# Performance work log

Hardware: AMD Instinct MI355X
Metric: run time of the kernel (lower is better)

The kernel has to match this reference:

```python
import jax, jax.numpy as jnp
import numpy as np

B, L, F, P = 128, 256, 4, 4   # dialogs, dialog length, future/past links
IN, H, C = 1024, 256, 7
N = B * L


def _build_edges():
    # same structure as build_intra_graph: self-loop + F future + P past per node
    i = np.arange(L)
    ss, tt = [], []
    for d in range(-P, F + 1):
        j = i + d
        m = (j >= 0) & (j < L)
        ss.append(i[m]); tt.append(j[m])
    s = np.concatenate(ss); t = np.concatenate(tt)
    offs = (np.arange(B) * L)[:, None]
    S = (s[None, :] + offs).ravel()
    T = (t[None, :] + offs).ravel()
    return np.stack([S, T]).astype(np.int32)


def setup_inputs() -> dict:
    key = jax.random.key(0)
    ks = jax.random.split(key, 16)
    ei = _build_edges()
    speakers = np.asarray(jax.random.randint(ks[0], (N,), 0, 2), dtype=np.int32)
    rel = (speakers[ei[0]] * speakers[ei[1]]).astype(np.int32)
    sd_in = 1.0 / np.sqrt(IN)
    sd_h = 1.0 / np.sqrt(H)
    return {
        "input": jax.random.normal(ks[1], (N, IN), jnp.float32),
        "dialog_lengths": jnp.full((B,), L, jnp.int32),
        "speakers": jnp.asarray(speakers),
        "labels": jax.random.randint(ks[2], (N,), 0, C, jnp.int32),
        "edge_index": jnp.asarray(ei),
        "rel_type": jnp.asarray(rel),
        # RGCNConv(IN, H, num_relations=2): per-relation weight, root weight, bias
        "W_rgcn": jax.random.normal(ks[3], (2, IN, H), jnp.float32) * sd_in,
        "W_root": jax.random.normal(ks[4], (IN, H), jnp.float32) * sd_in,
        "b_rgcn": jax.random.normal(ks[5], (H,), jnp.float32) * 0.01,
        # GraphConv(H, H): lin_rel (on aggregated neighbors, with bias), lin_root (no bias)
        "W_rel": jax.random.normal(ks[6], (H, H), jnp.float32) * sd_h,
        "b_rel": jax.random.normal(ks[7], (H,), jnp.float32) * 0.01,
        "W_grt": jax.random.normal(ks[8], (H, H), jnp.float32) * sd_h,
        # skip_con: Linear(IN, H)
        "W_skip": jax.random.normal(ks[9], (IN, H), jnp.float32) * sd_in,
        "b_skip": jax.random.normal(ks[10], (H,), jnp.float32) * 0.01,
        # classify: Linear(H, C)
        "W_cls": jax.random.normal(ks[11], (H, C), jnp.float32) * sd_h,
        "b_cls": jax.random.normal(ks[12], (C,), jnp.float32) * 0.01,
    }


def reference(input, dialog_lengths, speakers, labels, edge_index, rel_type,
              W_rgcn, W_root, b_rgcn, W_rel, b_rel, W_grt,
              W_skip, b_skip, W_cls, b_cls):
    n = input.shape[0]
    src, dst = edge_index[0], edge_index[1]
    seg = jax.ops.segment_sum

    # --- RGCNConv: out_i = x_i @ W_root + b + sum_r mean_{j in N_r(i)} x_j @ W_r
    t = jnp.einsum('ni,rio->rno', input, W_rgcn)      # [2, N, H]
    msg = t[rel_type, src]                            # [E, H] relation-specific messages
    h = input @ W_root + b_rgcn
    for r in range(2):
        m = (rel_type == r).astype(input.dtype)       # [E]
        s = seg(msg * m[:, None], dst, num_segments=n)
        cnt = seg(m, dst, num_segments=n)
        h = h + s / jnp.maximum(cnt, 1.0)[:, None]    # mean aggregation per relation

    # --- GraphConv (aggr='add'): out_i = W_rel @ sum_j h_j + b_rel + W_grt @ h_i
    neigh = seg(h[src], dst, num_segments=n)          # [N, H]
    h2 = neigh @ W_rel + b_rel + h @ W_grt

    # --- skip connection + classifier
    out = (h2 + input @ W_skip + b_skip) @ W_cls + b_cls  # [N, C]

    # --- cross entropy (mean)
    logp = jax.nn.log_softmax(out, axis=-1)
    loss = -jnp.mean(jnp.take_along_axis(logp, labels[:, None].astype(jnp.int32), axis=1))
    return out, loss
```

## Files before the change

### kernel.cpp

```cpp
#include <hip/hip_runtime.h>

#define NN 32768
#define INF 1024
#define HF 256

typedef __bf16 bf16x8 __attribute__((ext_vector_type(8)));
typedef float f32x4 __attribute__((ext_vector_type(4)));
typedef unsigned short u16x8 __attribute__((ext_vector_type(8)));

__device__ __forceinline__ float bf2f(unsigned short u) {
  union { unsigned int i; float f; } v; v.i = ((unsigned int)u) << 16; return v.f;
}
__device__ __forceinline__ unsigned short f2bf(float f) {
  union { float f; unsigned int i; } v; v.f = f;
  unsigned int x = v.i;
  return (unsigned short)((x + 0x7fffu + ((x >> 16) & 1u)) >> 16);
}

__device__ __forceinline__ void ld_lds16(const unsigned short* g, unsigned short* l) {
  __builtin_amdgcn_global_load_lds(
      (__attribute__((address_space(1))) const unsigned int*)g,
      (__attribute__((address_space(3))) unsigned int*)l, 16, 0, 0);
}

__global__ __launch_bounds__(256)
void diagcn_prep(const float* __restrict__ x, const float* __restrict__ Wrgcn,
                 const float* __restrict__ Wroot, const float* __restrict__ Wskip,
                 const float* __restrict__ Wgrt, const float* __restrict__ Wrel,
                 unsigned short* __restrict__ Xbf, unsigned short* __restrict__ WbigT,
                 unsigned short* __restrict__ WsmT, float* __restrict__ loss) {
  int bid = blockIdx.x;
  if (bid < 32768) {
    if (bid == 0 && threadIdx.x == 0) loss[0] = 0.f;
    int idx = bid * 256 + threadIdx.x;
    float4 v = ((const float4*)x)[idx];
    ushort4 u; u.x = f2bf(v.x); u.y = f2bf(v.y); u.z = f2bf(v.z); u.w = f2bf(v.w);
    ((ushort4*)Xbf)[idx] = u;
    return;
  }
  __shared__ float tile[64 * 65];
  int tb = bid - 32768;
  const float* src;
  int k0, ncol0;
  unsigned short* dst;
  int ldd, nrow0;
  if (tb < 256) {
    int tn = tb >> 4, tk = tb & 15;
    int mat = tn >> 2;
    src = (mat == 0) ? Wrgcn : (mat == 1) ? (Wrgcn + 262144) : (mat == 2) ? Wroot : Wskip;
    k0 = tk * 64; ncol0 = (tn & 3) * 64;
    dst = WbigT; ldd = 1024; nrow0 = tn * 64;
  } else {
    int t2 = tb - 256;
    int tn = t2 >> 3, tk = t2 & 7;
    src = (tk < 4) ? Wgrt : Wrel;
    k0 = (tk & 3) * 64; ncol0 = tn * 64;
    dst = WsmT; ldd = 512; nrow0 = tn * 64;
  }
  int kdst0 = (tb < 256) ? k0 : (((tb - 256) & 7) * 64);
  int c = threadIdx.x & 63, rb = threadIdx.x >> 6;
#pragma unroll
  for (int it = 0; it < 16; ++it) {
    int r = rb + it * 4;
    tile[r * 65 + c] = src[(size_t)(k0 + r) * 256 + ncol0 + c];
  }
  __syncthreads();
  int kk = threadIdx.x & 63;
#pragma unroll
  for (int it = 0; it < 16; ++it) {
    int nn = rb + it * 4;
    dst[(size_t)(nrow0 + nn) * ldd + kdst0 + kk] = f2bf(tile[kk * 65 + nn]);
  }
}

__global__ __launch_bounds__(256)
void diagcn_gemm1(const unsigned short* __restrict__ A, const unsigned short* __restrict__ BT,
                  unsigned short* __restrict__ Y) {
  const int K = 1024;
  __shared__ unsigned short As[128 * 64];
  __shared__ unsigned short Bs[128 * 64];
  const int tid = threadIdx.x;
  const int w = tid >> 6, lane = tid & 63;
  const int wm = w >> 1, wn = w & 1;
  const int quad = lane >> 4, l15 = lane & 15;
  const int b = blockIdx.x;
  const int m0 = (((b & 7) << 5) + (b >> 6)) << 7;
  const int n0 = ((b >> 3) & 7) << 7;
  const int rowg = lane >> 3;
  const int kbsw = (lane & 7) ^ rowg;

  f32x4 acc[4][4] = {};
  const unsigned short* Abase = A + (size_t)m0 * K + kbsw * 8;
  const unsigned short* Bbase = BT + (size_t)n0 * K + kbsw * 8;

  for (int k0 = 0; k0 < K; k0 += 64) {
#pragma unroll
    for (int t = 0; t < 4; ++t) {
      int grp = w * 4 + t;
      int rl = grp * 8 + rowg;
      ld_lds16(Abase + (size_t)rl * K + k0, &As[grp * 512]);
      ld_lds16(Bbase + (size_t)rl * K + k0, &Bs[grp * 512]);
    }
    __syncthreads();
#pragma unroll
    for (int ks = 0; ks < 2; ++ks) {
      bf16x8 av[4], bv[4];
      int kb = ks * 4 + quad;
#pragma unroll
      for (int i = 0; i < 4; ++i) {
        int ra = wm * 64 + i * 16 + l15;
        int rb2 = wn * 64 + i * 16 + l15;
        av[i] = *(const bf16x8*)&As[ra * 64 + ((kb ^ (ra & 7)) << 3)];
        bv[i] = *(const bf16x8*)&Bs[rb2 * 64 + ((kb ^ (rb2 & 7)) << 3)];
      }
#pragma unroll
      for (int i = 0; i < 4; ++i)
#pragma unroll
        for (int j = 0; j < 4; ++j)
          acc[i][j] = __builtin_amdgcn_mfma_f32_16x16x32_bf16(av[i], bv[j], acc[i][j], 0, 0, 0);
    }
    __syncthreads();
  }
#pragma unroll
  for (int i = 0; i < 4; ++i)
#pragma unroll
    for (int j = 0; j < 4; ++j) {
      int row = m0 + wm * 64 + i * 16 + quad * 4;
      int col = n0 + wn * 64 + j * 16 + l15;
#pragma unroll
      for (int r = 0; r < 4; ++r)
        Y[(size_t)(row + r) * 1024 + col] = f2bf(acc[i][j][r]);
    }
}

__global__ __launch_bounds__(256)
void diagcn_h(const unsigned short* __restrict__ Y, const int* __restrict__ spk,
              const float* __restrict__ brgcn, unsigned short* __restrict__ A2) {
  int b = blockIdx.x;
  int wv = threadIdx.x >> 6, lane = threadIdx.x & 63;
  int half = lane >> 5, li = lane & 31, c0 = li << 3;
  int node = ((b & 7) << 12) + ((b >> 3) << 3) + wv * 2 + half;
  int p = node & 255, dbase = node - p;
  int si = spk[node];
  float a0[8] = {}, a1[8] = {};
  float n0 = 0.f, n1 = 0.f;
#pragma unroll
  for (int d = -4; d <= 4; ++d) {
    int pj = p + d;
    float w = (pj >= 0 && pj < 256) ? 1.f : 0.f;
    int jc = pj < 0 ? 0 : (pj > 255 ? 255 : pj);
    int nj = dbase + jc;
    int rel = si & spk[nj];
    u16x8 v = *(const u16x8*)&Y[(size_t)nj * 1024 + (rel << 8) + c0];
    float w1 = rel ? w : 0.f, w0 = rel ? 0.f : w;
#pragma unroll
    for (int k = 0; k < 8; ++k) {
      float f = bf2f(v[k]);
      a0[k] += f * w0; a1[k] += f * w1;
    }
    n0 += w0; n1 += w1;
  }
  u16x8 vr = *(const u16x8*)&Y[(size_t)node * 1024 + 512 + c0];
  float i0 = 1.f / fmaxf(n0, 1.f), i1 = 1.f / fmaxf(n1, 1.f);
  u16x8 u;
#pragma unroll
  for (int k = 0; k < 8; ++k)
    u[k] = f2bf(bf2f(vr[k]) + brgcn[c0 + k] + a0[k] * i0 + a1[k] * i1);
  *(u16x8*)&A2[(size_t)node * 512 + c0] = u;
}

__global__ __launch_bounds__(256)
void diagcn_neigh(unsigned short* __restrict__ A2) {
  int b = blockIdx.x;
  int wv = threadIdx.x >> 6, lane = threadIdx.x & 63;
  int half = lane >> 5, li = lane & 31, c0 = li << 3;
  int node = ((b & 7) << 12) + ((b >> 3) << 3) + wv * 2 + half;
  int p = node & 255, dbase = node - p;
  float s[8] = {};
#pragma unroll
  for (int d = -4; d <= 4; ++d) {
    int pj = p + d;
    float w = (pj >= 0 && pj < 256) ? 1.f : 0.f;
    int jc = pj < 0 ? 0 : (pj > 255 ? 255 : pj);
    u16x8 v = *(const u16x8*)&A2[(size_t)(dbase + jc) * 512 + c0];
#pragma unroll
    for (int k = 0; k < 8; ++k) s[k] += bf2f(v[k]) * w;
  }
  u16x8 u;
#pragma unroll
  for (int k = 0; k < 8; ++k) u[k] = f2bf(s[k]);
  *(u16x8*)&A2[(size_t)node * 512 + 256 + c0] = u;
}

__global__ __launch_bounds__(256)
void diagcn_gemm2(const unsigned short* __restrict__ A, const unsigned short* __restrict__ BT,
                  const unsigned short* __restrict__ Y, const float* __restrict__ Wcls,
                  const float* __restrict__ bcls, const float* __restrict__ brel,
                  const float* __restrict__ bskip, const int* __restrict__ labels,
                  float* __restrict__ out, float* __restrict__ loss) {
  const int K = 512;
  __shared__ unsigned short As[64 * 64];
  __shared__ unsigned short Bs[256 * 64];
  __shared__ float Wc[2312];
  for (int i = threadIdx.x; i < 2312; i += 256) {
    float v;
    if (i < 1792) v = Wcls[i];
    else if (i < 1799) v = bcls[i - 1792];
    else if (i < 1800) v = 0.f;
    else if (i < 2056) v = brel[i - 1800];
    else v = bskip[i - 2056];
    Wc[i] = v;
  }
  const int tid = threadIdx.x;
  const int w = tid >> 6, lane = tid & 63;
  const int quad = lane >> 4, l15 = lane & 15;
  const int b = blockIdx.x;
  const int m0 = (((b & 7) << 6) + (b >> 3)) << 6;
  const int rowg = lane >> 3;
  const int kbsw = (lane & 7) ^ rowg;

  f32x4 acc[16] = {};
  const unsigned short* Abase = A + (size_t)m0 * K + kbsw * 8;
  const unsigned short* Bbase = BT + kbsw * 8;

  for (int k0 = 0; k0 < K; k0 += 64) {
#pragma unroll
    for (int t = 0; t < 2; ++t) {
      int grp = w * 2 + t;
      ld_lds16(Abase + (size_t)(grp * 8 + rowg) * K + k0, &As[grp * 512]);
    }
#pragma unroll
    for (int t = 0; t < 8; ++t) {
      int grp = w * 8 + t;
      ld_lds16(Bbase + (size_t)(grp * 8 + rowg) * K + k0, &Bs[grp * 512]);
    }
    __syncthreads();
#pragma unroll
    for (int ks = 0; ks < 2; ++ks) {
      int kb = ks * 4 + quad;
      int ra = w * 16 + l15;
      bf16x8 av = *(const bf16x8*)&As[ra * 64 + ((kb ^ (ra & 7)) << 3)];
#pragma unroll
      for (int j = 0; j < 16; ++j) {
        int rb2 = j * 16 + l15;
        bf16x8 bv = *(const bf16x8*)&Bs[rb2 * 64 + ((kb ^ (rb2 & 7)) << 3)];
        acc[j] = __builtin_amdgcn_mfma_f32_16x16x32_bf16(av, bv, acc[j], 0, 0, 0);
      }
    }
    __syncthreads();
  }

  float wsum[4][7] = {};
#pragma unroll
  for (int j = 0; j < 16; ++j) {
    int col = j * 16 + l15;
    float bb = Wc[1800 + col] + Wc[2056 + col];
#pragma unroll
    for (int r = 0; r < 4; ++r) {
      int row = m0 + w * 16 + quad * 4 + r;
      float z = acc[j][r] + bb + bf2f(Y[(size_t)row * 1024 + 768 + col]);
#pragma unroll
      for (int c = 0; c < 7; ++c) wsum[r][c] += z * Wc[col * 7 + c];
    }
  }
#pragma unroll
  for (int o = 1; o < 16; o <<= 1)
#pragma unroll
    for (int r = 0; r < 4; ++r)
#pragma unroll
      for (int c = 0; c < 7; ++c) wsum[r][c] += __shfl_xor(wsum[r][c], o, 64);

  float lsum = 0.f;
#pragma unroll
  for (int r = 0; r < 4; ++r) {
    int row = m0 + w * 16 + quad * 4 + r;
    float o7[7], mx = -1e30f;
#pragma unroll
    for (int c = 0; c < 7; ++c) {
      o7[c] = wsum[r][c] + Wc[1792 + c];
      mx = fmaxf(mx, o7[c]);
    }
    if (l15 < 7) out[(size_t)row * 7 + l15] = o7[l15];
    float s = 0.f;
#pragma unroll
    for (int c = 0; c < 7; ++c) s += expf(o7[c] - mx);
    int lab = labels[row];
    lsum += mx + logf(s) - o7[lab];
  }
  lsum += __shfl_xor(lsum, 16, 64);
  lsum += __shfl_xor(lsum, 32, 64);
  if (lane == 0) atomicAdd(loss, lsum * (1.0f / (float)NN));
}

extern "C" void kernel_launch(void* const* d_in, const int* in_sizes, int n_in,
                              void* d_out, int out_size, void* d_ws, size_t ws_size,
                              hipStream_t stream) {
  const float* x      = (const float*)d_in[0];
  const int* speakers = (const int*)d_in[2];
  const int* labels   = (const int*)d_in[3];
  const float* Wrgcn  = (const float*)d_in[6];
  const float* Wroot  = (const float*)d_in[7];
  const float* brgcn  = (const float*)d_in[8];
  const float* Wrel   = (const float*)d_in[9];
  const float* brel   = (const float*)d_in[10];
  const float* Wgrt   = (const float*)d_in[11];
  const float* Wskip  = (const float*)d_in[12];
  const float* bskip  = (const float*)d_in[13];
  const float* Wcls   = (const float*)d_in[14];
  const float* bcls   = (const float*)d_in[15];
  float* out = (float*)d_out;
  float* loss = out + (size_t)NN * 7;

  const size_t OFF_XBF  = 0;
  const size_t OFF_WBIG = 67108864;
  const size_t OFF_WSM  = 69206016;
  const size_t OFF_Y    = 69468160;
  const size_t OFF_A2   = 136577024;
  const size_t NEED     = 170131456;
  if (ws_size < NEED) return;

  char* ws = (char*)d_ws;
  unsigned short* Xbf   = (unsigned short*)(ws + OFF_XBF);
  unsigned short* WbigT = (unsigned short*)(ws + OFF_WBIG);
  unsigned short* WsmT  = (unsigned short*)(ws + OFF_WSM);
  unsigned short* Y     = (unsigned short*)(ws + OFF_Y);
  unsigned short* A2    = (unsigned short*)(ws + OFF_A2);

  diagcn_prep<<<dim3(33056), dim3(256), 0, stream>>>(x, Wrgcn, Wroot, Wskip, Wgrt, Wrel,
                                                     Xbf, WbigT, WsmT, loss);
  diagcn_gemm1<<<dim3(2048), dim3(256), 0, stream>>>(Xbf, WbigT, Y);
  diagcn_h<<<dim3(NN / 8), dim3(256), 0, stream>>>(Y, speakers, brgcn, A2);
  diagcn_neigh<<<dim3(NN / 8), dim3(256), 0, stream>>>(A2);
  diagcn_gemm2<<<dim3(512), dim3(256), 0, stream>>>(A2, WsmT, Y, Wcls, bcls, brel, bskip,
                                                    labels, out, loss);
}
```

Before: 379.5 us.

## Rewrite first GEMM as 256x256-tile, 8-wave, 4-stage LDS pipelined kernel

The big bf16 GEMM (32768x1024x1024) moves from 128x128 tiles with 4 waves and single-buffered LDS to 256x256 tiles with 8 waves and a 4-deep ring of K=32 LDS stages. Global-to-LDS loads for tile t+3 are issued in the middle of the MFMA work for tile t, and waits use explicit vmcnt counts and raw barriers. s_setprio is raised around the MFMA bursts. This aims to hide load latency and cut global traffic per FLOP, at the cost of 128KB of LDS per block, 128 accumulator registers per lane, and tricky hand-written synchronisation.

Result: no change. 372.2 us (-1.9%).

```diff
diff --git a/kernel.cpp b/kernel.cpp
--- a/kernel.cpp
+++ b/kernel.cpp
@@ -73,60 +73,109 @@
   }
 }
 
-__global__ __launch_bounds__(256)
+template<bool STG>
+__device__ __forceinline__ void g1_tile(int t,
+    const unsigned short* __restrict__ gA0, const unsigned short* __restrict__ gB0,
+    unsigned short* SH, int w, int abase, int bbase, int sw8,
+    f32x4 (&acc)[8][4]) {
+  unsigned short* Ab = SH + ((t & 3) << 14);
+  unsigned short* Bb = Ab + 8192;
+  bf16x8 av[4], bv[4];
+#pragma unroll
+  for (int i = 0; i < 4; ++i)
+    av[i] = *(const bf16x8*)&Ab[(abase + i * 16) * 32 + sw8];
+#pragma unroll
+  for (int j = 0; j < 4; ++j)
+    bv[j] = *(const bf16x8*)&Bb[(bbase + j * 16) * 32 + sw8];
+  if (STG) {
+    unsigned short* d = SH + (((t + 3) & 3) << 14) + (w << 10);
+    const unsigned short* g = gA0 + (t + 3) * 32;
+    ld_lds16(g, d);
+    ld_lds16(g + 16 * 1024, d + 512);
+  }
+  __builtin_amdgcn_s_barrier();
+  asm volatile("s_waitcnt lgkmcnt(0)");
+  __builtin_amdgcn_s_setprio(1);
+#pragma unroll
+  for (int i = 0; i < 4; ++i)
+#pragma unroll
+    for (int j = 0; j < 4; ++j)
+      acc[i][j] = __builtin_amdgcn_mfma_f32_16x16x32_bf16(av[i], bv[j], acc[i][j], 0, 0, 0);
+  __builtin_amdgcn_s_setprio(0);
+  __builtin_amdgcn_s_barrier();
+#pragma unroll
+  for (int i = 0; i < 4; ++i)
+    av[i] = *(const bf16x8*)&Ab[(abase + 64 + i * 16) * 32 + sw8];
+  if (STG) {
+    unsigned short* d = SH + (((t + 3) & 3) << 14) + 8192 + (w << 10);
+    const unsigned short* g = gB0 + (t + 3) * 32;
+    ld_lds16(g, d);
+    ld_lds16(g + 16 * 1024, d + 512);
+  }
+  __builtin_amdgcn_s_barrier();
+  asm volatile("s_waitcnt lgkmcnt(0)");
+  __builtin_amdgcn_s_setprio(1);
+#pragma unroll
+  for (int i = 0; i < 4; ++i)
+#pragma unroll
+    for (int j = 0; j < 4; ++j)
+      acc[4 + i][j] = __builtin_amdgcn_mfma_f32_16x16x32_bf16(av[i], bv[j], acc[4 + i][j], 0, 0, 0);
+  __builtin_amdgcn_s_setprio(0);
+}
+
+__global__ __launch_bounds__(512, 2)
 void diagcn_gemm1(const unsigned short* __restrict__ A, const unsigned short* __restrict__ BT,
                   unsigned short* __restrict__ Y) {
-  const int K = 1024;
-  __shared__ unsigned short As[128 * 64];
-  __shared__ unsigned short Bs[128 * 64];
+  __shared__ unsigned short SH[65536];
   const int tid = threadIdx.x;
   const int w = tid >> 6, lane = tid & 63;
-  const int wm = w >> 1, wn = w & 1;
   const int quad = lane >> 4, l15 = lane & 15;
+  const int wm = w >> 2, wn = w & 3;
   const int b = blockIdx.x;
-  const int m0 = (((b & 7) << 5) + (b >> 6)) << 7;
-  const int n0 = ((b >> 3) & 7) << 7;
-  const int rowg = lane >> 3;
-  const int kbsw = (lane & 7) ^ rowg;
-
-  f32x4 acc[4][4] = {};
-  const unsigned short* Abase = A + (size_t)m0 * K + kbsw * 8;
-  const unsigned short* Bbase = BT + (size_t)n0 * K + kbsw * 8;
-
-  for (int k0 = 0; k0 < K; k0 += 64) {
-#pragma unroll
-    for (int t = 0; t < 4; ++t) {
-      int grp = w * 4 + t;
-      int rl = grp * 8 + rowg;
-      ld_lds16(Abase + (size_t)rl * K + k0, &As[grp * 512]);
-      ld_lds16(Bbase + (size_t)rl * K + k0, &Bs[grp * 512]);
-    }
-    __syncthreads();
-#pragma unroll
-    for (int ks = 0; ks < 2; ++ks) {
-      bf16x8 av[4], bv[4];
-      int kb = ks * 4 + quad;
-#pragma unroll
-      for (int i = 0; i < 4; ++i) {
-        int ra = wm * 64 + i * 16 + l15;
-        int rb2 = wn * 64 + i * 16 + l15;
-        av[i] = *(const bf16x8*)&As[ra * 64 + ((kb ^ (ra & 7)) << 3)];
-        bv[i] = *(const bf16x8*)&Bs[rb2 * 64 + ((kb ^ (rb2 & 7)) << 3)];
-      }
-#pragma unroll
-      for (int i = 0; i < 4; ++i)
-#pragma unroll
-        for (int j = 0; j < 4; ++j)
-          acc[i][j] = __builtin_amdgcn_mfma_f32_16x16x32_bf16(av[i], bv[j], acc[i][j], 0, 0, 0);
-    }
-    __syncthreads();
-  }
-#pragma unroll
-  for (int i = 0; i < 4; ++i)
+  const int wg = ((b & 7) << 6) + (b >> 3);
+  const int m0 = (wg >> 2) << 8;
+  const int n0 = (wg & 3) << 8;
+  const int abase = wm * 128 + l15;
+  const int bbase = wn * 64 + l15;
+  const int sw8 = ((quad ^ ((l15 >> 1) & 3)) << 3);
+  const int csrc8 = (((lane & 3) ^ ((lane >> 3) & 3)) << 3);
+  const unsigned short* gA0 = A + (size_t)(m0 + w * 32 + (lane >> 2)) * 1024 + csrc8;
+  const unsigned short* gB0 = BT + (size_t)(n0 + w * 32 + (lane >> 2)) * 1024 + csrc8;
+
+  f32x4 acc[8][4] = {};
+
+#pragma unroll
+  for (int tt = 0; tt < 3; ++tt) {
+    unsigned short* dA = SH + (tt << 14) + (w << 10);
+    ld_lds16(gA0 + tt * 32, dA);
+    ld_lds16(gA0 + tt * 32 + 16 * 1024, dA + 512);
+    unsigned short* dB = SH + (tt << 14) + 8192 + (w << 10);
+    ld_lds16(gB0 + tt * 32, dB);
+    ld_lds16(gB0 + tt * 32 + 16 * 1024, dB + 512);
+  }
+  asm volatile("s_waitcnt vmcnt(8)" ::: "memory");
+  __builtin_amdgcn_s_barrier();
+
+#pragma unroll 1
+  for (int t = 0; t < 29; ++t) {
+    g1_tile<true>(t, gA0, gB0, SH, w, abase, bbase, sw8, acc);
+    asm volatile("s_waitcnt vmcnt(8)" ::: "memory");
+    __builtin_amdgcn_s_barrier();
+  }
+  g1_tile<false>(29, gA0, gB0, SH, w, abase, bbase, sw8, acc);
+  asm volatile("s_waitcnt vmcnt(4)" ::: "memory");
+  __builtin_amdgcn_s_barrier();
+  g1_tile<false>(30, gA0, gB0, SH, w, abase, bbase, sw8, acc);
+  asm volatile("s_waitcnt vmcnt(0)" ::: "memory");
+  __builtin_amdgcn_s_barrier();
+  g1_tile<false>(31, gA0, gB0, SH, w, abase, bbase, sw8, acc);
+
+#pragma unroll
+  for (int i = 0; i < 8; ++i)
 #pragma unroll
     for (int j = 0; j < 4; ++j) {
-      int row = m0 + wm * 64 + i * 16 + quad * 4;
-      int col = n0 + wn * 64 + j * 16 + l15;
+      const int row = m0 + wm * 128 + i * 16 + quad * 4;
+      const int col = n0 + wn * 64 + j * 16 + l15;
 #pragma unroll
       for (int r = 0; r < 4; ++r)
         Y[(size_t)(row + r) * 1024 + col] = f2bf(acc[i][j][r]);
@@ -328,7 +377,7 @@
 
   diagcn_prep<<<dim3(33056), dim3(256), 0, stream>>>(x, Wrgcn, Wroot, Wskip, Wgrt, Wrel,
                                                      Xbf, WbigT, WsmT, loss);
-  diagcn_gemm1<<<dim3(2048), dim3(256), 0, stream>>>(Xbf, WbigT, Y);
+  diagcn_gemm1<<<dim3(512), dim3(512), 0, stream>>>(Xbf, WbigT, Y);
   diagcn_h<<<dim3(NN / 8), dim3(256), 0, stream>>>(Y, speakers, brgcn, A2);
   diagcn_neigh<<<dim3(NN / 8), dim3(256), 0, stream>>>(A2);
   diagcn_gemm2<<<dim3(512), dim3(256), 0, stream>>>(A2, WsmT, Y, Wcls, bcls, brel, bskip,
```
